# Optimization experiments

Hardware: AMD Instinct MI355X
Metric: run time of the kernel (lower is better)

Reference implementation:

```python
import jax, jax.numpy as jnp
import numpy as np

N = 1_000_000   # number of input points
C = 32          # feature channels
S = 64          # spatial size per dim (and batch-key range)

def _linear_keys(coords):
    # coords: [N, 4] int32 -> unique int64 key per (x, y, z, batch)
    c = coords.astype(jnp.int64)
    return ((c[:, 0] * S + c[:, 1]) * S + c[:, 2]) * S + c[:, 3]

def setup_inputs() -> dict:
    key = jax.random.key(0)
    k1, k2 = jax.random.split(key)
    coords = jax.random.randint(k1, (N, 4), 0, S, dtype=jnp.int32)
    features = jax.random.normal(k2, (N, C), dtype=jnp.float32)
    return {"coords": coords, "features": features}

def reference(coords, features):
    # SCN InputLayer, mode=3 (sum duplicates): dedupe coordinate keys,
    # scatter-add features of duplicate points into the unique voxel row.
    keys = _linear_keys(coords)                       # [N] int64
    # fixed-size unique for jit compatibility; padding rows get no contributions
    _, inv = jnp.unique(keys, size=N, fill_value=-1, return_inverse=True)
    out = jax.ops.segment_sum(features, inv, num_segments=N)  # [N, C]
    return out
```

## Files before the change

kernel.cpp:

```cpp
#include <hip/hip_runtime.h>


constexpr int S = 64;
constexpr int KEYSPACE = S * S * S * S;
constexpr int NWORDS   = KEYSPACE / 32;
constexpr int SCAN_BLK = 256;
constexpr int NSCANBLK = NWORDS / SCAN_BLK;

__device__ __forceinline__ unsigned make_key(int4 c) {
    return (unsigned)(((c.x * S + c.y) * S + c.z) * S + c.w);
}

__global__ void k_setbits(const int4* __restrict__ coords,
                          unsigned* __restrict__ bitmap, int n) {
    int i = blockIdx.x * blockDim.x + threadIdx.x;
    if (i < n) {
        unsigned key = make_key(coords[i]);
        atomicOr(&bitmap[key >> 5], 1u << (key & 31));
    }
}

__global__ void k_blocksums(const unsigned* __restrict__ bitmap,
                            unsigned* __restrict__ blockSums) {
    int w = blockIdx.x * SCAN_BLK + threadIdx.x;
    unsigned pc = __popc(bitmap[w]);
    for (int off = 32; off > 0; off >>= 1) pc += __shfl_down(pc, off);
    __shared__ unsigned sm[SCAN_BLK / 64];
    if ((threadIdx.x & 63) == 0) sm[threadIdx.x >> 6] = pc;
    __syncthreads();
    if (threadIdx.x == 0) {
        unsigned s = 0;
        for (int j = 0; j < SCAN_BLK / 64; ++j) s += sm[j];
        blockSums[blockIdx.x] = s;
    }
}

__global__ void k_scan(const unsigned* __restrict__ blockSums,
                       unsigned* __restrict__ blockOffs) {
    __shared__ unsigned tsum[256];
    int t = threadIdx.x;
    unsigned v[8];
    unsigned s = 0;
    for (int j = 0; j < 8; ++j) { v[j] = blockSums[t * 8 + j]; s += v[j]; }
    tsum[t] = s;
    __syncthreads();
    unsigned pre = 0;
    for (int j = 0; j < t; ++j) pre += tsum[j];
    for (int j = 0; j < 8; ++j) { blockOffs[t * 8 + j] = pre; pre += v[j]; }
}

__global__ void k_wordprefix(const unsigned* __restrict__ bitmap,
                             const unsigned* __restrict__ blockOffs,
                             unsigned* __restrict__ wordPrefix) {
    int t = threadIdx.x;
    int w = blockIdx.x * SCAN_BLK + t;
    unsigned pc = __popc(bitmap[w]);
    __shared__ unsigned sm[SCAN_BLK];
    sm[t] = pc;
    __syncthreads();
    unsigned pre = 0;
    for (int j = 0; j < t; ++j) pre += sm[j];
    wordPrefix[w] = blockOffs[blockIdx.x] + pre;
}

__global__ void k_scatter(const int4* __restrict__ coords,
                          const float* __restrict__ feats,
                          const unsigned* __restrict__ bitmap,
                          const unsigned* __restrict__ wordPrefix,
                          float* __restrict__ out, int n) {
    long long gid = (long long)blockIdx.x * blockDim.x + threadIdx.x;
    int i = (int)(gid >> 5);
    int c = (int)(gid & 31);
    if (i >= n) return;
    unsigned key = make_key(coords[i]);
    unsigned w = key >> 5, bit = key & 31;
    unsigned rank = wordPrefix[w] + __popc(bitmap[w] & ((1u << bit) - 1u));
    atomicAdd(&out[(long long)rank * 32 + c], feats[(long long)i * 32 + c]);
}

extern "C" void kernel_launch(void* const* d_in, const int* in_sizes, int n_in,
                              void* d_out, int out_size, void* d_ws, size_t ws_size,
                              hipStream_t stream) {
    const int4*  coords = (const int4*)d_in[0];
    const float* feats  = (const float*)d_in[1];
    float* out = (float*)d_out;
    int n = in_sizes[0] / 4;

    unsigned* bitmap     = (unsigned*)d_ws;
    unsigned* wordPrefix = bitmap + NWORDS;
    unsigned* blockSums  = wordPrefix + NWORDS;
    unsigned* blockOffs  = blockSums + NSCANBLK;

    hipMemsetAsync(bitmap, 0, (size_t)NWORDS * sizeof(unsigned), stream);
    hipMemsetAsync(d_out, 0, (size_t)out_size * sizeof(float), stream);

    k_setbits<<<(n + 255) / 256, 256, 0, stream>>>(coords, bitmap, n);
    k_blocksums<<<NSCANBLK, SCAN_BLK, 0, stream>>>(bitmap, blockSums);
    k_scan<<<1, 256, 0, stream>>>(blockSums, blockOffs);
    k_wordprefix<<<NSCANBLK, SCAN_BLK, 0, stream>>>(bitmap, blockOffs, wordPrefix);

    long long tot = (long long)n * 32;
    k_scatter<<<(int)((tot + 255) / 256), 256, 0, stream>>>(
        coords, feats, bitmap, wordPrefix, out, n);
}
```

Before: 395.3 us.

## Split scatter into first-writer stores and atomic duplicates, drop full output memset

```diff
diff --git a/kernel.cpp b/kernel.cpp
--- a/kernel.cpp
+++ b/kernel.cpp
@@ -7,17 +7,16 @@
 constexpr int SCAN_BLK = 256;
 constexpr int NSCANBLK = NWORDS / SCAN_BLK;
 
-__device__ __forceinline__ unsigned make_key(int4 c) {
-    return (unsigned)(((c.x * S + c.y) * S + c.z) * S + c.w);
-}
-
 __global__ void k_setbits(const int4* __restrict__ coords,
-                          unsigned* __restrict__ bitmap, int n) {
+                          unsigned* __restrict__ bitmap,
+                          unsigned* __restrict__ keys, int n) {
     int i = blockIdx.x * blockDim.x + threadIdx.x;
-    if (i < n) {
-        unsigned key = make_key(coords[i]);
-        atomicOr(&bitmap[key >> 5], 1u << (key & 31));
-    }
+    if (i >= n) return;
+    int4 c = coords[i];
+    unsigned key = (unsigned)(((c.x * S + c.y) * S + c.z) * S + c.w);
+    unsigned bit = 1u << (key & 31);
+    unsigned old = atomicOr(&bitmap[key >> 5], bit);
+    keys[i] = key | ((old & bit) ? 0u : 0x80000000u);
 }
 
 __global__ void k_blocksums(const unsigned* __restrict__ bitmap,
@@ -36,7 +35,8 @@
 }
 
 __global__ void k_scan(const unsigned* __restrict__ blockSums,
-                       unsigned* __restrict__ blockOffs) {
+                       unsigned* __restrict__ blockOffs,
+                       unsigned* __restrict__ d_total) {
     __shared__ unsigned tsum[256];
     int t = threadIdx.x;
     unsigned v[8];
@@ -47,59 +47,100 @@
     unsigned pre = 0;
     for (int j = 0; j < t; ++j) pre += tsum[j];
     for (int j = 0; j < 8; ++j) { blockOffs[t * 8 + j] = pre; pre += v[j]; }
+    if (t == 255) d_total[0] = pre;
 }
 
-__global__ void k_wordprefix(const unsigned* __restrict__ bitmap,
-                             const unsigned* __restrict__ blockOffs,
-                             unsigned* __restrict__ wordPrefix) {
+__global__ void k_meta(const unsigned* __restrict__ bitmap,
+                       const unsigned* __restrict__ blockOffs,
+                       uint2* __restrict__ meta) {
     int t = threadIdx.x;
     int w = blockIdx.x * SCAN_BLK + t;
-    unsigned pc = __popc(bitmap[w]);
-    __shared__ unsigned sm[SCAN_BLK];
-    sm[t] = pc;
+    unsigned bits = bitmap[w];
+    unsigned pc = __popc(bits);
+    unsigned inc = pc;
+    for (int off = 1; off < 64; off <<= 1) {
+        unsigned x = __shfl_up(inc, off);
+        if ((t & 63) >= off) inc += x;
+    }
+    __shared__ unsigned wsum[SCAN_BLK / 64];
+    if ((t & 63) == 63) wsum[t >> 6] = inc;
     __syncthreads();
-    unsigned pre = 0;
-    for (int j = 0; j < t; ++j) pre += sm[j];
-    wordPrefix[w] = blockOffs[blockIdx.x] + pre;
+    unsigned base = 0;
+    for (int j = 0; j < (t >> 6); ++j) base += wsum[j];
+    meta[w] = make_uint2(bits, blockOffs[blockIdx.x] + base + (inc - pc));
 }
 
-__global__ void k_scatter(const int4* __restrict__ coords,
-                          const float* __restrict__ feats,
-                          const unsigned* __restrict__ bitmap,
-                          const unsigned* __restrict__ wordPrefix,
-                          float* __restrict__ out, int n) {
-    long long gid = (long long)blockIdx.x * blockDim.x + threadIdx.x;
-    int i = (int)(gid >> 5);
-    int c = (int)(gid & 31);
+__global__ void k_scatter1(const unsigned* __restrict__ keys,
+                           const float4* __restrict__ feats4,
+                           const uint2* __restrict__ meta,
+                           float4* __restrict__ out4, int n) {
+    int gid = blockIdx.x * blockDim.x + threadIdx.x;
+    int i = gid >> 3;
     if (i >= n) return;
-    unsigned key = make_key(coords[i]);
-    unsigned w = key >> 5, bit = key & 31;
-    unsigned rank = wordPrefix[w] + __popc(bitmap[w] & ((1u << bit) - 1u));
-    atomicAdd(&out[(long long)rank * 32 + c], feats[(long long)i * 32 + c]);
+    unsigned kw = keys[i];
+    if (!(kw & 0x80000000u)) return;
+    unsigned key = kw & 0x00FFFFFFu;
+    uint2 m = meta[key >> 5];
+    unsigned rank = m.y + __popc(m.x & ((1u << (key & 31)) - 1u));
+    int c4 = gid & 7;
+    out4[(long long)rank * 8 + c4] = feats4[(long long)i * 8 + c4];
+}
+
+__global__ void k_scatter2(const unsigned* __restrict__ keys,
+                           const float* __restrict__ feats,
+                           const uint2* __restrict__ meta,
+                           float* __restrict__ out, int n) {
+    int i = blockIdx.x * blockDim.x + threadIdx.x;
+    if (i >= n) return;
+    unsigned kw = keys[i];
+    if (kw & 0x80000000u) return;
+    unsigned key = kw & 0x00FFFFFFu;
+    uint2 m = meta[key >> 5];
+    unsigned rank = m.y + __popc(m.x & ((1u << (key & 31)) - 1u));
+    const float* f = feats + (long long)i * 32;
+    float* o = out + (long long)rank * 32;
+#pragma unroll
+    for (int c = 0; c < 32; ++c) atomicAdd(&o[c], f[c]);
+}
+
+__global__ void k_tailzero(float4* __restrict__ out4,
+                           const unsigned* __restrict__ d_total, int n) {
+    unsigned nU = *d_total;
+    long long start = (long long)nU * 8;
+    long long end   = (long long)n * 8;
+    long long stride = (long long)gridDim.x * blockDim.x;
+    for (long long idx = start + blockIdx.x * (long long)blockDim.x + threadIdx.x;
+         idx < end; idx += stride)
+        out4[idx] = make_float4(0.f, 0.f, 0.f, 0.f);
 }
 
 extern "C" void kernel_launch(void* const* d_in, const int* in_sizes, int n_in,
                               void* d_out, int out_size, void* d_ws, size_t ws_size,
                               hipStream_t stream) {
-    const int4*  coords = (const int4*)d_in[0];
-    const float* feats  = (const float*)d_in[1];
-    float* out = (float*)d_out;
+    const int4*   coords = (const int4*)d_in[0];
+    const float*  feats  = (const float*)d_in[1];
+    const float4* feats4 = (const float4*)d_in[1];
+    float*  out  = (float*)d_out;
+    float4* out4 = (float4*)d_out;
     int n = in_sizes[0] / 4;
+    if (n <= 0) return;
 
-    unsigned* bitmap     = (unsigned*)d_ws;
-    unsigned* wordPrefix = bitmap + NWORDS;
-    unsigned* blockSums  = wordPrefix + NWORDS;
-    unsigned* blockOffs  = blockSums + NSCANBLK;
+    unsigned* bitmap    = (unsigned*)d_ws;
+    uint2*    meta      = (uint2*)(bitmap + NWORDS);
+    unsigned* keys      = bitmap + NWORDS + 2 * NWORDS;
+    unsigned* blockSums = keys + n;
+    unsigned* blockOffs = blockSums + NSCANBLK;
+    unsigned* d_total   = blockOffs + NSCANBLK;
 
     hipMemsetAsync(bitmap, 0, (size_t)NWORDS * sizeof(unsigned), stream);
-    hipMemsetAsync(d_out, 0, (size_t)out_size * sizeof(float), stream);
 
-    k_setbits<<<(n + 255) / 256, 256, 0, stream>>>(coords, bitmap, n);
+    k_setbits<<<(n + 255) / 256, 256, 0, stream>>>(coords, bitmap, keys, n);
     k_blocksums<<<NSCANBLK, SCAN_BLK, 0, stream>>>(bitmap, blockSums);
-    k_scan<<<1, 256, 0, stream>>>(blockSums, blockOffs);
-    k_wordprefix<<<NSCANBLK, SCAN_BLK, 0, stream>>>(bitmap, blockOffs, wordPrefix);
+    k_scan<<<1, 256, 0, stream>>>(blockSums, blockOffs, d_total);
+    k_meta<<<NSCANBLK, SCAN_BLK, 0, stream>>>(bitmap, blockOffs, meta);
 
-    long long tot = (long long)n * 32;
-    k_scatter<<<(int)((tot + 255) / 256), 256, 0, stream>>>(
-        coords, feats, bitmap, wordPrefix, out, n);
+    long long lanes = (long long)n * 8;
+    k_scatter1<<<(int)((lanes + 255) / 256), 256, 0, stream>>>(keys, feats4, meta, out4, n);
+    k_scatter2<<<(n + 255) / 256, 256, 0, stream>>>(keys, feats, meta, out, n);
+    k_tailzero<<<512, 256, 0, stream>>>(out4, d_total, n);
 }
```

After: 341.0 us. 1.16x faster.
